# Performance work log

Hardware: AMD Instinct MI355X
Metric: run time of the kernel (lower is better)

Reference implementation:

```python
import jax, jax.numpy as jnp
import numpy as np

EPS = 1e-6
N_HEADS, N_KV = 16, 4


def rmsnorm(x, w):
    return x * jax.lax.rsqrt(jnp.mean(x * x, axis=-1, keepdims=True) + EPS) * w


def setup_inputs() -> dict:
    key = jax.random.key(0)
    ks = jax.random.split(key, 9)
    B, T, D, F = 2, 2048, 2048, 8192
    KVD = N_KV * (D // N_HEADS)
    s = lambda k, shape, fan: (jax.random.normal(k, shape, jnp.float32) * (fan ** -0.5))
    return {
        "x": jax.random.normal(ks[0], (B, T, D), jnp.float32),
        "norm1_w": jnp.ones((D,), jnp.float32),
        "norm2_w": jnp.ones((D,), jnp.float32),
        "Wq": s(ks[1], (D, D), D),
        "Wk": s(ks[2], (D, KVD), D),
        "Wv": s(ks[3], (D, KVD), D),
        "Wo": s(ks[4], (D, D), D),
        "Wc": s(ks[5], (D, D), D),
        "W1": s(ks[6], (D, F), D),
        "W2": s(ks[7], (F, D), F),
        "W3": s(ks[8], (D, F), D),
    }


def reference(x, norm1_w, norm2_w, Wq, Wk, Wv, Wo, Wc, W1, W2, W3):
    B, T, D = x.shape
    dh = D // N_HEADS          # 128
    G = N_HEADS // N_KV        # groups per kv head
    scale = dh ** -0.5

    xn = rmsnorm(x, norm1_w)
    q = xn @ Wq                               # [B,T,D]
    pos = q @ Wc                              # CoPE stand-in: contextual positional bias on Q
    q = (q + pos).reshape(B, T, N_KV, G, dh)  # group q heads under their kv head
    k = (xn @ Wk).reshape(B, T, N_KV, dh)
    v = (xn @ Wv).reshape(B, T, N_KV, dh)

    # GQA without repeat_interleave: contract each group against shared K/V
    scores = jnp.einsum('bqkgd,bskd->bkgqs', q, k) * scale   # [B,KV,G,T,T]
    i = jnp.arange(T)
    causal = i[:, None] >= i[None, :]
    scores = jnp.where(causal, scores, -jnp.inf)
    w = jax.nn.softmax(scores, axis=-1)
    att = jnp.einsum('bkgqs,bskd->bqkgd', w, v).reshape(B, T, D)

    x = x + att @ Wo
    xn2 = rmsnorm(x, norm2_w)
    x = x + (jax.nn.silu(xn2 @ W1) * (xn2 @ W3)) @ W2
    return x
```

## Files before the change

### kernel.cpp

```cpp
#include <hip/hip_runtime.h>
#include <hip/hip_bf16.h>

typedef __attribute__((ext_vector_type(8))) short short8;
typedef __attribute__((ext_vector_type(4))) float floatx4;
typedef unsigned short ushort_t;

__device__ inline float b2f(ushort_t s) {
    return __uint_as_float(((unsigned int)s) << 16);
}
__device__ inline ushort_t f2b(float f) {
    unsigned int u = __float_as_uint(f);
    unsigned int r = 0x7fff + ((u >> 16) & 1);
    return (ushort_t)((u + r) >> 16);
}
__device__ inline void load8(const float* p, float* f) {
    float4 a = *(const float4*)p;
    float4 b = *(const float4*)(p + 4);
    f[0] = a.x; f[1] = a.y; f[2] = a.z; f[3] = a.w;
    f[4] = b.x; f[5] = b.y; f[6] = b.z; f[7] = b.w;
}
__device__ inline void gload16(const ushort_t* g, ushort_t* l) {
    __builtin_amdgcn_global_load_lds(
        (const __attribute__((address_space(1))) unsigned int*)g,
        (__attribute__((address_space(3))) unsigned int*)l, 16, 0, 0);
}

__global__ __launch_bounds__(256) void transpose_w(const float* __restrict__ src,
                                                   ushort_t* __restrict__ dst,
                                                   int K, int N) {
    __shared__ ushort_t tile[64][65];
    int kb = blockIdx.x * 64, nb = blockIdx.y * 64;
    int t = threadIdx.x;
#pragma unroll
    for (int i = 0; i < 4; ++i) {
        int r = (t >> 4) + i * 16;
        int c = (t & 15) * 4;
        float4 v = *(const float4*)(src + (size_t)(kb + r) * N + nb + c);
        tile[c + 0][r] = f2b(v.x);
        tile[c + 1][r] = f2b(v.y);
        tile[c + 2][r] = f2b(v.z);
        tile[c + 3][r] = f2b(v.w);
    }
    __syncthreads();
#pragma unroll
    for (int i = 0; i < 2; ++i) {
        int s = t + i * 256;
        int n = s >> 3, kc = (s & 7) * 8;
        ushort_t o[8];
#pragma unroll
        for (int j = 0; j < 8; ++j) o[j] = tile[n][kc + j];
        *(uint4*)(dst + (size_t)(nb + n) * K + kb + kc) = *(const uint4*)o;
    }
}

__global__ __launch_bounds__(256) void rmsnorm_kernel(const float* __restrict__ x,
                                                      const float* __restrict__ w,
                                                      ushort_t* __restrict__ out, int D) {
    int row = blockIdx.x;
    int t = threadIdx.x;
    const float* xr = x + (size_t)row * D;
    float f[8];
    load8(xr + t * 8, f);
    float ss = 0.f;
#pragma unroll
    for (int i = 0; i < 8; ++i) ss += f[i] * f[i];
#pragma unroll
    for (int m = 1; m < 64; m <<= 1) ss += __shfl_xor(ss, m);
    __shared__ float wsum[4];
    if ((t & 63) == 0) wsum[t >> 6] = ss;
    __syncthreads();
    float tot = wsum[0] + wsum[1] + wsum[2] + wsum[3];
    float r = rsqrtf(tot / (float)D + 1e-6f);
    float wf[8];
    load8(w + t * 8, wf);
    ushort_t o[8];
#pragma unroll
    for (int i = 0; i < 8; ++i) o[i] = f2b(f[i] * r * wf[i]);
    *(uint4*)(out + (size_t)row * D + t * 8) = *(const uint4*)o;
}

__global__ __launch_bounds__(256) void reduce_out(const ushort_t* __restrict__ p,
                                                  const float* __restrict__ resid,
                                                  float* __restrict__ out, int n) {
    int stride = gridDim.x * 256;
    for (int i = blockIdx.x * 256 + threadIdx.x; i * 8 < n; i += stride) {
        int i8 = i * 8;
        uint4 a = *(const uint4*)(p + i8);
        uint4 b = *(const uint4*)(p + n + i8);
        const ushort_t* ae = (const ushort_t*)&a;
        const ushort_t* be = (const ushort_t*)&b;
        float rr[8];
        load8(resid + i8, rr);
        float o[8];
#pragma unroll
        for (int j = 0; j < 8; ++j) o[j] = b2f(ae[j]) + b2f(be[j]) + rr[j];
        *(float4*)(out + i8) = make_float4(o[0], o[1], o[2], o[3]);
        *(float4*)(out + i8 + 4) = make_float4(o[4], o[5], o[6], o[7]);
    }
}

__device__ inline void vm6() { asm volatile("s_waitcnt vmcnt(6)" ::: "memory"); }
__device__ inline void vm4() { asm volatile("s_waitcnt vmcnt(4)" ::: "memory"); }

template <int MODE>
__global__ __launch_bounds__(512, 2) void gemm8(const ushort_t* __restrict__ A,
                                                const ushort_t* __restrict__ Bt,
                                                const ushort_t* __restrict__ aux,
                                                const float* __restrict__ aux2,
                                                void* __restrict__ Cv,
                                                void* __restrict__ C2v,
                                                void* __restrict__ C3v,
                                                int M, int N, int Ksub, int lda) {
    __shared__ __align__(16) ushort_t Lds[2 * 32768];
    const int tid = threadIdx.x;
    const int wv = tid >> 6, lane = tid & 63;
    const int l16 = lane & 15, l4 = lane >> 4;
    const int wr = wv >> 2, wc = wv & 3;
    int nwg = gridDim.x;
    int per = nwg >> 3;
    int wg = (blockIdx.x & 7) * per + (blockIdx.x >> 3);
    int mtiles = M >> 8;
    int bx = wg & (mtiles - 1);
    int by = wg / mtiles;
    int bm = bx << 8, bn = by << 8;
    int koff = blockIdx.y * Ksub;

    const int sr = tid >> 3;
    const int scol = (((tid & 7) ^ (sr & 7)) << 3);
    const ushort_t* gA = A + (size_t)(bm + sr) * lda + scol + koff;
    const ushort_t* gB = Bt + (size_t)(bn + sr) * lda + scol + koff;
    ushort_t* ldsw = Lds + wv * 512;

    const int ktiles = Ksub >> 6;
    const int niter = ktiles >> 1;
    const int km = ktiles - 1;

#define STG_A(slot, j, kt) gload16(gA + (size_t)((j) * 64) * lda + ((kt) << 6), ldsw + (slot) * 32768 + (j) * 4096)
#define STG_B(slot, j, kt) gload16(gB + (size_t)((j) * 64) * lda + ((kt) << 6), ldsw + (slot) * 32768 + 16384 + (j) * 4096)

    STG_A(0, 0, 0); STG_A(0, 2, 0); STG_A(0, 1, 0); STG_A(0, 3, 0);
    STG_B(0, 0, 0); STG_B(0, 1, 0); STG_B(0, 2, 0); STG_B(0, 3, 0);
    STG_A(1, 0, 1); STG_A(1, 2, 1);
    STG_B(1, 0, 1); STG_B(1, 1, 1); STG_B(1, 2, 1); STG_B(1, 3, 1);
    vm6();
    asm volatile("" ::: "memory");
    __builtin_amdgcn_s_barrier();

    const int lx = l4 ^ (l16 & 7);
    floatx4 acc[8][4] = {};
    short8 aR[4][2], bR[4][2];

#define DSA(slot, mh) { _Pragma("unroll") for (int m = 0; m < 4; ++m) { \
    _Pragma("unroll") for (int kk = 0; kk < 2; ++kk) \
      aR[m][kk] = *(const short8*)(Lds + (slot) * 32768 + \
          (wr * 128 + (mh) * 64 + m * 16 + l16) * 64 + ((lx ^ (kk << 2)) << 3)); } }
#define DSB(slot, nh) { _Pragma("unroll") for (int n = 0; n < 2; ++n) { \
    _Pragma("unroll") for (int kk = 0; kk < 2; ++kk) \
      bR[(nh) * 2 + n][kk] = *(const short8*)(Lds + (slot) * 32768 + 16384 + \
          (wc * 64 + ((nh) * 2 + n) * 16 + l16) * 64 + ((lx ^ (kk << 2)) << 3)); } }
#define QUAD(mh, nlo) { _Pragma("unroll") for (int m = 0; m < 4; ++m) \
    _Pragma("unroll") for (int n = 0; n < 2; ++n) \
    _Pragma("unroll") for (int kk = 0; kk < 2; ++kk) \
      acc[(mh) * 4 + m][(nlo) + n] = __builtin_amdgcn_mfma_f32_16x16x32_bf16( \
          aR[m][kk], bR[(nlo) + n][kk], acc[(mh) * 4 + m][(nlo) + n], 0, 0, 0); }
#define PHASE(DS, ST, MH, NLO, VM) { \
    DS; ST; \
    asm volatile("" ::: "memory"); \
    __builtin_amdgcn_s_barrier(); \
    asm volatile("s_waitcnt lgkmcnt(0)" ::: "memory"); \
    __builtin_amdgcn_sched_barrier(0); \
    __builtin_amdgcn_s_setprio(1); \
    QUAD(MH, NLO); \
    __builtin_amdgcn_s_setprio(0); \
    VM; \
    asm volatile("" ::: "memory"); \
    __builtin_amdgcn_s_barrier(); }

    for (int it = 0; it < niter; ++it) {
        int t1 = 2 * it + 1;
        int t2 = (2 * it + 2) & km;
        int t3 = (2 * it + 3) & km;
        PHASE({ DSA(0, 0); DSB(0, 0); }, { STG_A(1, 1, t1); STG_A(1, 3, t1); }, 0, 0, );
        PHASE({ DSB(0, 1); },            { STG_A(0, 0, t2); STG_A(0, 2, t2); }, 0, 2, );
        PHASE({ DSA(0, 1); },            { STG_B(0, 0, t2); STG_B(0, 1, t2); }, 1, 2, );
        PHASE({ },                       { STG_B(0, 2, t2); STG_B(0, 3, t2); }, 1, 0, vm6(); );
        PHASE({ DSA(1, 0); DSB(1, 0); }, { STG_A(0, 1, t2); STG_A(0, 3, t2); }, 0, 0, );
        PHASE({ DSB(1, 1); },            { STG_A(1, 0, t3); STG_A(1, 2, t3); }, 0, 2, );
        PHASE({ DSA(1, 1); },            { STG_B(1, 0, t3); STG_B(1, 1, t3); }, 1, 2, );
        PHASE({ },                       { STG_B(1, 2, t3); STG_B(1, 3, t3); }, 1, 0, vm6(); );
    }

#pragma unroll
    for (int mi = 0; mi < 8; ++mi)
#pragma unroll
        for (int ni = 0; ni < 4; ++ni)
#pragma unroll
            for (int r = 0; r < 4; ++r) {
                int row = bm + wr * 128 + mi * 16 + l4 * 4 + r;
                int col = bn + wc * 64 + ni * 16 + l16;
                size_t idx = (size_t)row * N + col;
                float v = acc[mi][ni][r];
                if (MODE == 0) {
                    ((ushort_t*)Cv)[idx] = f2b(v);
                } else if (MODE == 1) {
                    ((ushort_t*)Cv)[idx] = f2b(v + b2f(aux[idx]));
                } else if (MODE == 2) {
                    float h = b2f(aux[idx]);
                    ((ushort_t*)Cv)[idx] = f2b((h / (1.f + __expf(-h))) * v);
                } else if (MODE == 3) {
                    ((ushort_t*)Cv)[(size_t)blockIdx.y * M * N + idx] = f2b(v);
                } else if (MODE == 5) {
                    ((float*)Cv)[idx] = v + aux2[idx];
                } else if (MODE == 6) {
                    if (bn < 2048) {
                        ((ushort_t*)Cv)[(size_t)row * 2048 + col] = f2b(v);
                    } else if (bn < 2560) {
                        ((ushort_t*)C2v)[(size_t)row * 512 + (col - 2048)] = f2b(v);
                    } else {
                        ((ushort_t*)C3v)[(size_t)(col - 2560) * 4096 + row] = f2b(v);
                    }
                }
            }
#undef STG_A
#undef STG_B
#undef DSA
#undef DSB
#undef QUAD
#undef PHASE
}

template <int MODE>
__global__ __launch_bounds__(512, 1) void gemm8h(const ushort_t* __restrict__ A,
                                                 const ushort_t* __restrict__ Bt,
                                                 const ushort_t* __restrict__ aux,
                                                 const float* __restrict__ aux2,
                                                 void* __restrict__ Cv,
                                                 int M, int N, int K) {
    __shared__ __align__(16) ushort_t Lds[2 * 24576];
    const int tid = threadIdx.x;
    const int wv = tid >> 6, lane = tid & 63;
    const int l16 = lane & 15, l4 = lane >> 4;
    const int wr = wv >> 2, wc = wv & 3;
    int nwg = gridDim.x;
    int per = nwg >> 3;
    int wg = (blockIdx.x & 7) * per + (blockIdx.x >> 3);
    int mtiles = M >> 7;
    int bx = wg & (mtiles - 1);
    int by = wg / mtiles;
    int bm = bx << 7, bn = by << 8;

    const int sr = tid >> 3;
    const int scol = (((tid & 7) ^ (sr & 7)) << 3);
    const ushort_t* gA = A + (size_t)(bm + sr) * K + scol;
    const ushort_t* gB = Bt + (size_t)(bn + sr) * K + scol;
    ushort_t* ldsw = Lds + wv * 512;

    const int ktiles = K >> 6;
    const int niter = ktiles >> 1;
    const int km = ktiles - 1;

#define HSTG_A(slot, j, kt) gload16(gA + (size_t)((j) * 64) * K + ((kt) << 6), ldsw + (slot) * 24576 + (j) * 4096)
#define HSTG_B(slot, j, kt) gload16(gB + (size_t)((j) * 64) * K + ((kt) << 6), ldsw + (slot) * 24576 + 8192 + (j) * 4096)

    HSTG_A(0, 0, 0); HSTG_A(0, 1, 0);
    HSTG_B(0, 0, 0); HSTG_B(0, 1, 0); HSTG_B(0, 2, 0); HSTG_B(0, 3, 0);
    HSTG_A(1, 0, 1); HSTG_A(1, 1, 1);
    HSTG_B(1, 0, 1); HSTG_B(1, 1, 1);
    vm4();
    asm volatile("" ::: "memory");
    __builtin_amdgcn_s_barrier();

    const int lx = l4 ^ (l16 & 7);
    floatx4 acc[4][4] = {};
    short8 aR[2][2], bR[4][2];

#define HDSA(slot, mh) { _Pragma("unroll") for (int m = 0; m < 2; ++m) { \
    _Pragma("unroll") for (int kk = 0; kk < 2; ++kk) \
      aR[m][kk] = *(const short8*)(Lds + (slot) * 24576 + \
          (wr * 64 + (mh) * 32 + m * 16 + l16) * 64 + ((lx ^ (kk << 2)) << 3)); } }
#define HDSB(slot, nh) { _Pragma("unroll") for (int n = 0; n < 2; ++n) { \
    _Pragma("unroll") for (int kk = 0; kk < 2; ++kk) \
      bR[(nh) * 2 + n][kk] = *(const short8*)(Lds + (slot) * 24576 + 8192 + \
          (wc * 64 + ((nh) * 2 + n) * 16 + l16) * 64 + ((lx ^ (kk << 2)) << 3)); } }
#define HQUAD(mh, nlo) { _Pragma("unroll") for (int m = 0; m < 2; ++m) \
    _Pragma("unroll") for (int n = 0; n < 2; ++n) \
    _Pragma("unroll") for (int kk = 0; kk < 2; ++kk) \
      acc[(mh) * 2 + m][(nlo) + n] = __builtin_amdgcn_mfma_f32_16x16x32_bf16( \
          aR[m][kk], bR[(nlo) + n][kk], acc[(mh) * 2 + m][(nlo) + n], 0, 0, 0); }
#define HPHASE(DS, ST, MH, NLO, VM) { \
    DS; ST; \
    asm volatile("" ::: "memory"); \
    __builtin_amdgcn_s_barrier(); \
    asm volatile("s_waitcnt lgkmcnt(0)" ::: "memory"); \
    __builtin_amdgcn_sched_barrier(0); \
    __builtin_amdgcn_s_setprio(1); \
    HQUAD(MH, NLO); \
    __builtin_amdgcn_s_setprio(0); \
    VM; \
    asm volatile("" ::: "memory"); \
    __builtin_amdgcn_s_barrier(); }

    for (int it = 0; it < niter; ++it) {
        int t1 = 2 * it + 1;
        int t2 = (2 * it + 2) & km;
        int t3 = (2 * it + 3) & km;
        HPHASE({ HDSA(0, 0); HDSB(0, 0); }, { HSTG_B(1, 2, t1); HSTG_B(1, 3, t1); }, 0, 0, );
        HPHASE({ HDSB(0, 1); },             { },                                     0, 2, );
        HPHASE({ HDSA(0, 1); },             { HSTG_B(0, 0, t2); HSTG_B(0, 1, t2); }, 1, 2, );
        HPHASE({ },                         { HSTG_B(0, 2, t2); HSTG_B(0, 3, t2); }, 1, 0, vm4(); );
        HPHASE({ HDSA(1, 0); HDSB(1, 0); }, { HSTG_A(0, 0, t2); HSTG_A(0, 1, t2); }, 0, 0, );
        HPHASE({ HDSB(1, 1); },             { },                                     0, 2, );
        HPHASE({ HDSA(1, 1); },             { HSTG_B(1, 0, t3); HSTG_B(1, 1, t3); }, 1, 2, );
        HPHASE({ },                         { HSTG_A(1, 0, t3); HSTG_A(1, 1, t3); }, 1, 0, vm4(); );
    }

#pragma unroll
    for (int mi = 0; mi < 4; ++mi)
#pragma unroll
        for (int ni = 0; ni < 4; ++ni)
#pragma unroll
            for (int r = 0; r < 4; ++r) {
                int row = bm + wr * 64 + mi * 16 + l4 * 4 + r;
                int col = bn + wc * 64 + ni * 16 + l16;
                size_t idx = (size_t)row * N + col;
                float v = acc[mi][ni][r];
                if (MODE == 1) ((ushort_t*)Cv)[idx] = f2b(v + b2f(aux[idx]));
                else if (MODE == 5) ((float*)Cv)[idx] = v + aux2[idx];
            }
#undef HSTG_A
#undef HSTG_B
#undef HDSA
#undef HDSB
#undef HQUAD
#undef HPHASE
}

#define QB 64
#define SB 64

__global__ __launch_bounds__(256, 2) void attn_kernel(const ushort_t* __restrict__ Q,
                                                      const ushort_t* __restrict__ Kb,
                                                      const ushort_t* __restrict__ VbT,
                                                      ushort_t* __restrict__ O, int Tlen) {
    const int D = 2048, KVD = 512, dh = 128;
    const int MTOK = 4096;
    int p = blockIdx.x, h = blockIdx.y, b = blockIdx.z;
    int kv = h >> 2;
    int t = threadIdx.x, wave = t >> 6, lane = t & 63;
    int l16 = lane & 15, l4 = lane >> 4;
    __shared__ __align__(16) ushort_t Ks[SB][dh + 8];
    __shared__ __align__(16) ushort_t Vt[dh][SB + 8];
    __shared__ __align__(16) ushort_t Ps[4][16][SB + 8];
    const float scale = 0.08838834764831845f;
    const ushort_t* Kg = Kb + ((size_t)(b * Tlen) + (t >> 4)) * KVD + kv * dh + (t & 15) * 8;
    const ushort_t* Vg = VbT + (size_t)(kv * dh + (t >> 3)) * MTOK + b * Tlen + (t & 7) * 8;

    for (int side = 0; side < 2; ++side) {
        int qt = side ? p : (31 - p);
        int qbase = qt * QB;
        int qfrag = qbase + wave * 16;
        short8 qf[4];
        const ushort_t* Qrow = Q + ((size_t)(b * Tlen) + qfrag + l16) * D + h * dh;
#pragma unroll
        for (int kk = 0; kk < 4; ++kk) qf[kk] = *(const short8*)(Qrow + kk * 32 + l4 * 8);
        floatx4 o_acc[8] = {};
        float m_r[4], l_r[4];
#pragma unroll
        for (int r = 0; r < 4; ++r) { m_r[r] = -INFINITY; l_r[r] = 0.f; }
        int nst = qt + 1;
        uint4 kreg[4], vreg[4];
#pragma unroll
        for (int p4 = 0; p4 < 4; ++p4) {
            kreg[p4] = *(const uint4*)(Kg + (size_t)(p4 * 16) * KVD);
            vreg[p4] = *(const uint4*)(Vg + (size_t)(p4 * 32) * MTOK);
        }
        for (int st = 0; st < nst; ++st) {
            __syncthreads();
#pragma unroll
            for (int p4 = 0; p4 < 4; ++p4) {
                *(uint4*)(&Ks[(t >> 4) + p4 * 16][(t & 15) * 8]) = kreg[p4];
                *(uint4*)(&Vt[(t >> 3) + p4 * 32][(t & 7) * 8]) = vreg[p4];
            }
            __syncthreads();
            if (st + 1 < nst) {
                size_t off = (size_t)(st + 1) * SB;
#pragma unroll
                for (int p4 = 0; p4 < 4; ++p4) {
                    kreg[p4] = *(const uint4*)(Kg + (off + p4 * 16) * KVD);
                    vreg[p4] = *(const uint4*)(Vg + (size_t)(p4 * 32) * MTOK + off);
                }
            }
            int s0 = st * SB;
            floatx4 sa[4] = {};
            __builtin_amdgcn_s_setprio(1);
#pragma unroll
            for (int ss = 0; ss < 4; ++ss)
#pragma unroll
                for (int kk = 0; kk < 4; ++kk) {
                    short8 kf = *(const short8*)(&Ks[ss * 16 + l16][kk * 32 + l4 * 8]);
                    sa[ss] = __builtin_amdgcn_mfma_f32_16x16x32_bf16(qf[kk], kf, sa[ss], 0, 0, 0);
                }
            __builtin_amdgcn_s_setprio(0);
            float sv[4][4], pmax[4];
#pragma unroll
            for (int r = 0; r < 4; ++r) pmax[r] = -INFINITY;
#pragma unroll
            for (int ss = 0; ss < 4; ++ss) {
                int scol = s0 + ss * 16 + l16;
#pragma unroll
                for (int r = 0; r < 4; ++r) {
                    int qrow = qfrag + l4 * 4 + r;
                    float v = sa[ss][r] * scale;
                    if (scol > qrow) v = -INFINITY;
                    sv[ss][r] = v;
                    pmax[r] = fmaxf(pmax[r], v);
                }
            }
#pragma unroll
            for (int m = 1; m < 16; m <<= 1)
#pragma unroll
                for (int r = 0; r < 4; ++r) pmax[r] = fmaxf(pmax[r], __shfl_xor(pmax[r], m));
            int cflag = 1;
#pragma unroll
            for (int r = 0; r < 4; ++r) cflag &= (pmax[r] <= m_r[r] + 8.f) ? 1 : 0;
            bool skip = __all(cflag);
            float mn[4], rsum[4];
#pragma unroll
            for (int r = 0; r < 4; ++r) {
                mn[r] = skip ? m_r[r] : fmaxf(m_r[r], pmax[r]);
                rsum[r] = 0.f;
            }
#pragma unroll
            for (int ss = 0; ss < 4; ++ss)
#pragma unroll
                for (int r = 0; r < 4; ++r) {
                    float pv = __expf(sv[ss][r] - mn[r]);
                    sv[ss][r] = pv;
                    rsum[r] += pv;
                }
#pragma unroll
            for (int m = 1; m < 16; m <<= 1)
#pragma unroll
                for (int r = 0; r < 4; ++r) rsum[r] += __shfl_xor(rsum[r], m);
            if (skip) {
#pragma unroll
                for (int r = 0; r < 4; ++r) l_r[r] += rsum[r];
            } else {
#pragma unroll
                for (int r = 0; r < 4; ++r) {
                    float esc = __expf(m_r[r] - mn[r]);
                    l_r[r] = l_r[r] * esc + rsum[r];
                    m_r[r] = mn[r];
#pragma unroll
                    for (int c = 0; c < 8; ++c) o_acc[c][r] *= esc;
                }
            }
#pragma unroll
            for (int ss = 0; ss < 4; ++ss)
#pragma unroll
                for (int r = 0; r < 4; ++r)
                    Ps[wave][l4 * 4 + r][ss * 16 + l16] = f2b(sv[ss][r]);
            short8 pa[2];
#pragma unroll
            for (int kk = 0; kk < 2; ++kk)
                pa[kk] = *(const short8*)(&Ps[wave][l16][kk * 32 + l4 * 8]);
            __builtin_amdgcn_s_setprio(1);
#pragma unroll
            for (int c = 0; c < 8; ++c)
#pragma unroll
                for (int kk = 0; kk < 2; ++kk) {
                    short8 vf = *(const short8*)(&Vt[c * 16 + l16][kk * 32 + l4 * 8]);
                    o_acc[c] = __builtin_amdgcn_mfma_f32_16x16x32_bf16(pa[kk], vf, o_acc[c], 0, 0, 0);
                }
            __builtin_amdgcn_s_setprio(0);
        }
        __syncthreads();
        ushort_t* Osh = &Ks[0][0];
#pragma unroll
        for (int c = 0; c < 8; ++c)
#pragma unroll
            for (int r = 0; r < 4; ++r)
                Osh[(wave * 16 + l4 * 4 + r) * 136 + c * 16 + l16] = f2b(o_acc[c][r] / l_r[r]);
        __syncthreads();
        {
            int orow = t >> 2, occ = (t & 3) * 32;
            const ushort_t* srcp = Osh + orow * 136 + occ;
            ushort_t* dstp = O + ((size_t)(b * Tlen) + qbase + orow) * D + h * dh + occ;
#pragma unroll
            for (int k = 0; k < 4; ++k)
                *(uint4*)(dstp + k * 8) = *(const uint4*)(srcp + k * 8);
        }
    }
}

extern "C" void kernel_launch(void* const* d_in, const int* in_sizes, int n_in,
                              void* d_out, int out_size, void* d_ws, size_t ws_size,
                              hipStream_t stream) {
    const float* x   = (const float*)d_in[0];
    const float* n1w = (const float*)d_in[1];
    const float* n2w = (const float*)d_in[2];
    const float* Wq  = (const float*)d_in[3];
    const float* Wk  = (const float*)d_in[4];
    const float* Wv  = (const float*)d_in[5];
    const float* Wo  = (const float*)d_in[6];
    const float* Wc  = (const float*)d_in[7];
    const float* W1  = (const float*)d_in[8];
    const float* W2  = (const float*)d_in[9];
    const float* W3  = (const float*)d_in[10];
    float* out = (float*)d_out;

    const int B = 2, T = 2048, D = 2048, F = 8192, KVD = 512;
    const int M = B * T;
    const size_t XD   = (size_t)M * D * 2;
    const size_t XDF  = (size_t)M * D * 4;
    const size_t KVSZ = (size_t)M * KVD * 2;
    const size_t MF   = (size_t)M * F * 2;
    const size_t WDD  = (size_t)D * D * 2;
    const size_t WQKV = (size_t)(D + 2 * KVD) * D * 2;
    const size_t WDF  = (size_t)D * F * 2;

    char* w = (char*)d_ws;
    ushort_t* xn    = (ushort_t*)(w);
    ushort_t* qtmp  = (ushort_t*)(w + XD);
    ushort_t* qfin  = (ushort_t*)(w + 2 * XD);
    float*    x2f   = (float*)   (w + 3 * XD);
    ushort_t* kbuf  = (ushort_t*)(w + 3 * XD + XDF);
    ushort_t* vbufT = (ushort_t*)(w + 3 * XD + XDF + KVSZ);
    ushort_t* h1    = (ushort_t*)(w + 3 * XD + XDF + 2 * KVSZ);
    char* wt = w + 3 * XD + XDF + 2 * KVSZ + MF;
    ushort_t* WqkvT = (ushort_t*)(wt);
    ushort_t* WcT   = (ushort_t*)(wt + WQKV);
    ushort_t* WoT   = (ushort_t*)(wt + WQKV + WDD);
    ushort_t* W1T   = (ushort_t*)(wt + WQKV + 2 * WDD);
    ushort_t* W3T   = (ushort_t*)(wt + WQKV + 2 * WDD + WDF);
    ushort_t* W2T   = (ushort_t*)(wt + WQKV + 2 * WDD + 2 * WDF);

    dim3 blk(256);
    dim3 blk8(512);

    transpose_w<<<dim3(D / 64, D / 64), blk, 0, stream>>>(Wq, WqkvT, D, D);
    transpose_w<<<dim3(D / 64, KVD / 64), blk, 0, stream>>>(Wk, WqkvT + (size_t)2048 * D, D, KVD);
    transpose_w<<<dim3(D / 64, KVD / 64), blk, 0, stream>>>(Wv, WqkvT + (size_t)2560 * D, D, KVD);
    transpose_w<<<dim3(D / 64, D / 64), blk, 0, stream>>>(Wc, WcT, D, D);
    transpose_w<<<dim3(D / 64, D / 64), blk, 0, stream>>>(Wo, WoT, D, D);
    transpose_w<<<dim3(D / 64, F / 64), blk, 0, stream>>>(W1, W1T, D, F);
    transpose_w<<<dim3(D / 64, F / 64), blk, 0, stream>>>(W3, W3T, D, F);
    transpose_w<<<dim3(F / 64, D / 64), blk, 0, stream>>>(W2, W2T, F, D);

    rmsnorm_kernel<<<M, blk, 0, stream>>>(x, n1w, xn, D);
    gemm8<6><<<dim3((M / 256) * (3072 / 256)), blk8, 0, stream>>>(
        xn, WqkvT, nullptr, nullptr, qtmp, kbuf, vbufT, M, 3072, D, D);
    gemm8h<1><<<dim3((M / 128) * (D / 256)), blk8, 0, stream>>>(
        qtmp, WcT, qtmp, nullptr, qfin, M, D, D);
    attn_kernel<<<dim3(16, 16, B), blk, 0, stream>>>(qfin, kbuf, vbufT, qtmp, T);
    gemm8h<5><<<dim3((M / 128) * (D / 256)), blk8, 0, stream>>>(
        qtmp, WoT, nullptr, x, x2f, M, D, D);
    rmsnorm_kernel<<<M, blk, 0, stream>>>(x2f, n2w, xn, D);
    gemm8<0><<<dim3((M / 256) * (F / 256)), blk8, 0, stream>>>(
        xn, W1T, nullptr, nullptr, h1, nullptr, nullptr, M, F, D, D);
    gemm8<2><<<dim3((M / 256) * (F / 256)), blk8, 0, stream>>>(
        xn, W3T, h1, nullptr, h1, nullptr, nullptr, M, F, D, D);
    gemm8<3><<<dim3((M / 256) * (D / 256), 2), blk8, 0, stream>>>(
        h1, W2T, nullptr, nullptr, xn, nullptr, nullptr, M, D, F / 2, F);
    reduce_out<<<1024, blk, 0, stream>>>(xn, x2f, out, M * D);
}
```

Baseline: 837.2 us.

## Process paired causal q-tiles together in attention and merge weight transposes

The attention kernel now handles the high and low query tiles of each block in one pass over K/V, so each K/V tile is loaded into LDS once and used for both query tiles while they overlap. This removes the second K/V streaming pass and doubles the MFMA work per loaded tile, at the cost of more registers (two sets of accumulators and Q fragments) and a larger P buffer in shared memory. Separately, the eight weight-transpose launches are merged into one kernel that dispatches on block index, which cuts launch overhead.

After: 851.0 us. Within noise of the previous version (+1.7%).

```diff
diff --git a/kernel.cpp b/kernel.cpp
--- a/kernel.cpp
+++ b/kernel.cpp
@@ -25,11 +25,26 @@
         (__attribute__((address_space(3))) unsigned int*)l, 16, 0, 0);
 }
 
-__global__ __launch_bounds__(256) void transpose_w(const float* __restrict__ src,
-                                                   ushort_t* __restrict__ dst,
-                                                   int K, int N) {
+__global__ __launch_bounds__(256) void transpose_all(
+    const float* __restrict__ s0, const float* __restrict__ s1,
+    const float* __restrict__ s2, const float* __restrict__ s3,
+    const float* __restrict__ s4, const float* __restrict__ s5,
+    const float* __restrict__ s6, const float* __restrict__ s7,
+    ushort_t* d0, ushort_t* d1, ushort_t* d2, ushort_t* d3,
+    ushort_t* d4, ushort_t* d5, ushort_t* d6, ushort_t* d7) {
+    int id = blockIdx.x;
+    const float* src; ushort_t* dst; int K, N;
+    if (id < 1024)       { src = s0; dst = d0; K = 2048; N = 2048; }
+    else if (id < 1280)  { id -= 1024;  src = s1; dst = d1; K = 2048; N = 512; }
+    else if (id < 1536)  { id -= 1280;  src = s2; dst = d2; K = 2048; N = 512; }
+    else if (id < 2560)  { id -= 1536;  src = s3; dst = d3; K = 2048; N = 2048; }
+    else if (id < 3584)  { id -= 2560;  src = s4; dst = d4; K = 2048; N = 2048; }
+    else if (id < 7680)  { id -= 3584;  src = s5; dst = d5; K = 2048; N = 8192; }
+    else if (id < 11776) { id -= 7680;  src = s6; dst = d6; K = 2048; N = 8192; }
+    else                 { id -= 11776; src = s7; dst = d7; K = 8192; N = 2048; }
+    int tn = N >> 6;
+    int kb = (id / tn) * 64, nb = (id % tn) * 64;
     __shared__ ushort_t tile[64][65];
-    int kb = blockIdx.x * 64, nb = blockIdx.y * 64;
     int t = threadIdx.x;
 #pragma unroll
     for (int i = 0; i < 4; ++i) {
@@ -338,6 +353,56 @@
 #define QB 64
 #define SB 64
 
+#define SOFTMAX_SIDE(sacc, m_r, l_r, o_acc, qfrag, psr)                         \
+    {                                                                           \
+        float sv[4][4], pmax[4];                                                \
+        _Pragma("unroll") for (int r = 0; r < 4; ++r) pmax[r] = -INFINITY;      \
+        _Pragma("unroll") for (int ss = 0; ss < 4; ++ss) {                      \
+            int scol = s0 + ss * 16 + l16;                                      \
+            _Pragma("unroll") for (int r = 0; r < 4; ++r) {                     \
+                int qrow = (qfrag) + l4 * 4 + r;                                \
+                float v = sacc[ss][r] * scale;                                  \
+                if (scol > qrow) v = -INFINITY;                                 \
+                sv[ss][r] = v;                                                  \
+                pmax[r] = fmaxf(pmax[r], v);                                    \
+            }                                                                   \
+        }                                                                       \
+        _Pragma("unroll") for (int m = 1; m < 16; m <<= 1)                      \
+            _Pragma("unroll") for (int r = 0; r < 4; ++r)                       \
+                pmax[r] = fmaxf(pmax[r], __shfl_xor(pmax[r], m));               \
+        int cflag = 1;                                                          \
+        _Pragma("unroll") for (int r = 0; r < 4; ++r)                           \
+            cflag &= (pmax[r] <= m_r[r] + 8.f) ? 1 : 0;                         \
+        bool skip = __all(cflag);                                               \
+        float mn[4], rsum[4];                                                   \
+        _Pragma("unroll") for (int r = 0; r < 4; ++r) {                         \
+            mn[r] = skip ? m_r[r] : fmaxf(m_r[r], pmax[r]);                     \
+            rsum[r] = 0.f;                                                      \
+        }                                                                       \
+        _Pragma("unroll") for (int ss = 0; ss < 4; ++ss)                        \
+            _Pragma("unroll") for (int r = 0; r < 4; ++r) {                     \
+                float pv = __expf(sv[ss][r] - mn[r]);                           \
+                sv[ss][r] = pv;                                                 \
+                rsum[r] += pv;                                                  \
+            }                                                                   \
+        _Pragma("unroll") for (int m = 1; m < 16; m <<= 1)                      \
+            _Pragma("unroll") for (int r = 0; r < 4; ++r)                       \
+                rsum[r] += __shfl_xor(rsum[r], m);                              \
+        if (skip) {                                                             \
+            _Pragma("unroll") for (int r = 0; r < 4; ++r) l_r[r] += rsum[r];    \
+        } else {                                                                \
+            _Pragma("unroll") for (int r = 0; r < 4; ++r) {                     \
+                float esc = __expf(m_r[r] - mn[r]);                             \
+                l_r[r] = l_r[r] * esc + rsum[r];                                \
+                m_r[r] = mn[r];                                                 \
+                _Pragma("unroll") for (int c = 0; c < 8; ++c) o_acc[c][r] *= esc; \
+            }                                                                   \
+        }                                                                       \
+        _Pragma("unroll") for (int ss = 0; ss < 4; ++ss)                        \
+            _Pragma("unroll") for (int r = 0; r < 4; ++r)                       \
+                Ps[psr][l4 * 4 + r][ss * 16 + l16] = f2b(sv[ss][r]);            \
+    }
+
 __global__ __launch_bounds__(256, 2) void attn_kernel(const ushort_t* __restrict__ Q,
                                                       const ushort_t* __restrict__ Kb,
                                                       const ushort_t* __restrict__ VbT,
@@ -350,146 +415,137 @@
     int l16 = lane & 15, l4 = lane >> 4;
     __shared__ __align__(16) ushort_t Ks[SB][dh + 8];
     __shared__ __align__(16) ushort_t Vt[dh][SB + 8];
-    __shared__ __align__(16) ushort_t Ps[4][16][SB + 8];
+    __shared__ __align__(16) ushort_t Ps[8][16][SB + 8];
     const float scale = 0.08838834764831845f;
     const ushort_t* Kg = Kb + ((size_t)(b * Tlen) + (t >> 4)) * KVD + kv * dh + (t & 15) * 8;
     const ushort_t* Vg = VbT + (size_t)(kv * dh + (t >> 3)) * MTOK + b * Tlen + (t & 7) * 8;
 
-    for (int side = 0; side < 2; ++side) {
-        int qt = side ? p : (31 - p);
-        int qbase = qt * QB;
-        int qfrag = qbase + wave * 16;
-        short8 qf[4];
-        const ushort_t* Qrow = Q + ((size_t)(b * Tlen) + qfrag + l16) * D + h * dh;
-#pragma unroll
-        for (int kk = 0; kk < 4; ++kk) qf[kk] = *(const short8*)(Qrow + kk * 32 + l4 * 8);
-        floatx4 o_acc[8] = {};
-        float m_r[4], l_r[4];
-#pragma unroll
-        for (int r = 0; r < 4; ++r) { m_r[r] = -INFINITY; l_r[r] = 0.f; }
-        int nst = qt + 1;
-        uint4 kreg[4], vreg[4];
+    int qt_hi = 31 - p, qt_lo = p;
+    int qbase_hi = qt_hi * QB, qbase_lo = qt_lo * QB;
+    int qfrag_hi = qbase_hi + wave * 16;
+    int qfrag_lo = qbase_lo + wave * 16;
+    short8 qh[4], ql[4];
+    {
+        const ushort_t* Qh = Q + ((size_t)(b * Tlen) + qfrag_hi + l16) * D + h * dh;
+        const ushort_t* Ql = Q + ((size_t)(b * Tlen) + qfrag_lo + l16) * D + h * dh;
+#pragma unroll
+        for (int kk = 0; kk < 4; ++kk) {
+            qh[kk] = *(const short8*)(Qh + kk * 32 + l4 * 8);
+            ql[kk] = *(const short8*)(Ql + kk * 32 + l4 * 8);
+        }
+    }
+    floatx4 oh[8] = {}, ol[8] = {};
+    float mh[4], lh[4], ml[4], ll[4];
+#pragma unroll
+    for (int r = 0; r < 4; ++r) { mh[r] = -INFINITY; lh[r] = 0.f; ml[r] = -INFINITY; ll[r] = 0.f; }
+    int nst = qt_hi + 1;
+    uint4 kreg[4], vreg[4];
+#pragma unroll
+    for (int p4 = 0; p4 < 4; ++p4) {
+        kreg[p4] = *(const uint4*)(Kg + (size_t)(p4 * 16) * KVD);
+        vreg[p4] = *(const uint4*)(Vg + (size_t)(p4 * 32) * MTOK);
+    }
+    for (int st = 0; st < nst; ++st) {
+        __syncthreads();
 #pragma unroll
         for (int p4 = 0; p4 < 4; ++p4) {
-            kreg[p4] = *(const uint4*)(Kg + (size_t)(p4 * 16) * KVD);
-            vreg[p4] = *(const uint4*)(Vg + (size_t)(p4 * 32) * MTOK);
+            *(uint4*)(&Ks[(t >> 4) + p4 * 16][(t & 15) * 8]) = kreg[p4];
+            *(uint4*)(&Vt[(t >> 3) + p4 * 32][(t & 7) * 8]) = vreg[p4];
         }
-        for (int st = 0; st < nst; ++st) {
-            __syncthreads();
+        __syncthreads();
+        if (st + 1 < nst) {
+            size_t off = (size_t)(st + 1) * SB;
 #pragma unroll
             for (int p4 = 0; p4 < 4; ++p4) {
-                *(uint4*)(&Ks[(t >> 4) + p4 * 16][(t & 15) * 8]) = kreg[p4];
-                *(uint4*)(&Vt[(t >> 3) + p4 * 32][(t & 7) * 8]) = vreg[p4];
+                kreg[p4] = *(const uint4*)(Kg + (off + p4 * 16) * KVD);
+                vreg[p4] = *(const uint4*)(Vg + (size_t)(p4 * 32) * MTOK + off);
             }
-            __syncthreads();
-            if (st + 1 < nst) {
-                size_t off = (size_t)(st + 1) * SB;
-#pragma unroll
-                for (int p4 = 0; p4 < 4; ++p4) {
-                    kreg[p4] = *(const uint4*)(Kg + (off + p4 * 16) * KVD);
-                    vreg[p4] = *(const uint4*)(Vg + (size_t)(p4 * 32) * MTOK + off);
-                }
-            }
-            int s0 = st * SB;
-            floatx4 sa[4] = {};
-            __builtin_amdgcn_s_setprio(1);
+        }
+        int s0 = st * SB;
+        bool dual = (st <= qt_lo);
+        floatx4 sh[4] = {}, sl[4] = {};
+        __builtin_amdgcn_s_setprio(1);
+        if (dual) {
 #pragma unroll
             for (int ss = 0; ss < 4; ++ss)
 #pragma unroll
                 for (int kk = 0; kk < 4; ++kk) {
                     short8 kf = *(const short8*)(&Ks[ss * 16 + l16][kk * 32 + l4 * 8]);
-                    sa[ss] = __builtin_amdgcn_mfma_f32_16x16x32_bf16(qf[kk], kf, sa[ss], 0, 0, 0);
+                    sh[ss] = __builtin_amdgcn_mfma_f32_16x16x32_bf16(qh[kk], kf, sh[ss], 0, 0, 0);
+                    sl[ss] = __builtin_amdgcn_mfma_f32_16x16x32_bf16(ql[kk], kf, sl[ss], 0, 0, 0);
                 }
-            __builtin_amdgcn_s_setprio(0);
-            float sv[4][4], pmax[4];
-#pragma unroll
-            for (int r = 0; r < 4; ++r) pmax[r] = -INFINITY;
-#pragma unroll
-            for (int ss = 0; ss < 4; ++ss) {
-                int scol = s0 + ss * 16 + l16;
-#pragma unroll
-                for (int r = 0; r < 4; ++r) {
-                    int qrow = qfrag + l4 * 4 + r;
-                    float v = sa[ss][r] * scale;
-                    if (scol > qrow) v = -INFINITY;
-                    sv[ss][r] = v;
-                    pmax[r] = fmaxf(pmax[r], v);
+        } else {
+#pragma unroll
+            for (int ss = 0; ss < 4; ++ss)
+#pragma unroll
+                for (int kk = 0; kk < 4; ++kk) {
+                    short8 kf = *(const short8*)(&Ks[ss * 16 + l16][kk * 32 + l4 * 8]);
+                    sh[ss] = __builtin_amdgcn_mfma_f32_16x16x32_bf16(qh[kk], kf, sh[ss], 0, 0, 0);
                 }
-            }
-#pragma unroll
-            for (int m = 1; m < 16; m <<= 1)
-#pragma unroll
-                for (int r = 0; r < 4; ++r) pmax[r] = fmaxf(pmax[r], __shfl_xor(pmax[r], m));
-            int cflag = 1;
-#pragma unroll
-            for (int r = 0; r < 4; ++r) cflag &= (pmax[r] <= m_r[r] + 8.f) ? 1 : 0;
-            bool skip = __all(cflag);
-            float mn[4], rsum[4];
-#pragma unroll
-            for (int r = 0; r < 4; ++r) {
-                mn[r] = skip ? m_r[r] : fmaxf(m_r[r], pmax[r]);
-                rsum[r] = 0.f;
-            }
-#pragma unroll
-            for (int ss = 0; ss < 4; ++ss)
-#pragma unroll
-                for (int r = 0; r < 4; ++r) {
-                    float pv = __expf(sv[ss][r] - mn[r]);
-                    sv[ss][r] = pv;
-                    rsum[r] += pv;
-                }
-#pragma unroll
-            for (int m = 1; m < 16; m <<= 1)
-#pragma unroll
-                for (int r = 0; r < 4; ++r) rsum[r] += __shfl_xor(rsum[r], m);
-            if (skip) {
-#pragma unroll
-                for (int r = 0; r < 4; ++r) l_r[r] += rsum[r];
-            } else {
-#pragma unroll
-                for (int r = 0; r < 4; ++r) {
-                    float esc = __expf(m_r[r] - mn[r]);
-                    l_r[r] = l_r[r] * esc + rsum[r];
-                    m_r[r] = mn[r];
-#pragma unroll
-                    for (int c = 0; c < 8; ++c) o_acc[c][r] *= esc;
-                }
-            }
-#pragma unroll
-            for (int ss = 0; ss < 4; ++ss)
-#pragma unroll
-                for (int r = 0; r < 4; ++r)
-                    Ps[wave][l4 * 4 + r][ss * 16 + l16] = f2b(sv[ss][r]);
-            short8 pa[2];
+        }
+        __builtin_amdgcn_s_setprio(0);
+        SOFTMAX_SIDE(sh, mh, lh, oh, qfrag_hi, wave)
+        if (dual) SOFTMAX_SIDE(sl, ml, ll, ol, qfrag_lo, wave + 4)
+        short8 pah[2], pal[2];
+#pragma unroll
+        for (int kk = 0; kk < 2; ++kk)
+            pah[kk] = *(const short8*)(&Ps[wave][l16][kk * 32 + l4 * 8]);
+        if (dual) {
 #pragma unroll
             for (int kk = 0; kk < 2; ++kk)
-                pa[kk] = *(const short8*)(&Ps[wave][l16][kk * 32 + l4 * 8]);
-            __builtin_amdgcn_s_setprio(1);
+                pal[kk] = *(const short8*)(&Ps[wave + 4][l16][kk * 32 + l4 * 8]);
+        }
+        __builtin_amdgcn_s_setprio(1);
+        if (dual) {
 #pragma unroll
             for (int c = 0; c < 8; ++c)
 #pragma unroll
                 for (int kk = 0; kk < 2; ++kk) {
                     short8 vf = *(const short8*)(&Vt[c * 16 + l16][kk * 32 + l4 * 8]);
-                    o_acc[c] = __builtin_amdgcn_mfma_f32_16x16x32_bf16(pa[kk], vf, o_acc[c], 0, 0, 0);
+                    oh[c] = __builtin_amdgcn_mfma_f32_16x16x32_bf16(pah[kk], vf, oh[c], 0, 0, 0);
+                    ol[c] = __builtin_amdgcn_mfma_f32_16x16x32_bf16(pal[kk], vf, ol[c], 0, 0, 0);
                 }
-            __builtin_amdgcn_s_setprio(0);
+        } else {
+#pragma unroll
+            for (int c = 0; c < 8; ++c)
+#pragma unroll
+                for (int kk = 0; kk < 2; ++kk) {
+                    short8 vf = *(const short8*)(&Vt[c * 16 + l16][kk * 32 + l4 * 8]);
+                    oh[c] = __builtin_amdgcn_mfma_f32_16x16x32_bf16(pah[kk], vf, oh[c], 0, 0, 0);
+                }
         }
-        __syncthreads();
-        ushort_t* Osh = &Ks[0][0];
-#pragma unroll
-        for (int c = 0; c < 8; ++c)
-#pragma unroll
-            for (int r = 0; r < 4; ++r)
-                Osh[(wave * 16 + l4 * 4 + r) * 136 + c * 16 + l16] = f2b(o_acc[c][r] / l_r[r]);
-        __syncthreads();
-        {
-            int orow = t >> 2, occ = (t & 3) * 32;
-            const ushort_t* srcp = Osh + orow * 136 + occ;
-            ushort_t* dstp = O + ((size_t)(b * Tlen) + qbase + orow) * D + h * dh + occ;
-#pragma unroll
-            for (int k = 0; k < 4; ++k)
-                *(uint4*)(dstp + k * 8) = *(const uint4*)(srcp + k * 8);
-        }
+        __builtin_amdgcn_s_setprio(0);
+    }
+    ushort_t* Osh = &Ks[0][0];
+    __syncthreads();
+#pragma unroll
+    for (int c = 0; c < 8; ++c)
+#pragma unroll
+        for (int r = 0; r < 4; ++r)
+            Osh[(wave * 16 + l4 * 4 + r) * 136 + c * 16 + l16] = f2b(oh[c][r] / lh[r]);
+    __syncthreads();
+    {
+        int orow = t >> 2, occ = (t & 3) * 32;
+        const ushort_t* srcp = Osh + orow * 136 + occ;
+        ushort_t* dstp = O + ((size_t)(b * Tlen) + qbase_hi + orow) * D + h * dh + occ;
+#pragma unroll
+        for (int k = 0; k < 4; ++k)
+            *(uint4*)(dstp + k * 8) = *(const uint4*)(srcp + k * 8);
+    }
+    __syncthreads();
+#pragma unroll
+    for (int c = 0; c < 8; ++c)
+#pragma unroll
+        for (int r = 0; r < 4; ++r)
+            Osh[(wave * 16 + l4 * 4 + r) * 136 + c * 16 + l16] = f2b(ol[c][r] / ll[r]);
+    __syncthreads();
+    {
+        int orow = t >> 2, occ = (t & 3) * 32;
+        const ushort_t* srcp = Osh + orow * 136 + occ;
+        ushort_t* dstp = O + ((size_t)(b * Tlen) + qbase_lo + orow) * D + h * dh + occ;
+#pragma unroll
+        for (int k = 0; k < 4; ++k)
+            *(uint4*)(dstp + k * 8) = *(const uint4*)(srcp + k * 8);
     }
 }
 
@@ -538,14 +594,10 @@
     dim3 blk(256);
     dim3 blk8(512);
 
-    transpose_w<<<dim3(D / 64, D / 64), blk, 0, stream>>>(Wq, WqkvT, D, D);
-    transpose_w<<<dim3(D / 64, KVD / 64), blk, 0, stream>>>(Wk, WqkvT + (size_t)2048 * D, D, KVD);
-    transpose_w<<<dim3(D / 64, KVD / 64), blk, 0, stream>>>(Wv, WqkvT + (size_t)2560 * D, D, KVD);
-    transpose_w<<<dim3(D / 64, D / 64), blk, 0, stream>>>(Wc, WcT, D, D);
-    transpose_w<<<dim3(D / 64, D / 64), blk, 0, stream>>>(Wo, WoT, D, D);
-    transpose_w<<<dim3(D / 64, F / 64), blk, 0, stream>>>(W1, W1T, D, F);
-    transpose_w<<<dim3(D / 64, F / 64), blk, 0, stream>>>(W3, W3T, D, F);
-    transpose_w<<<dim3(F / 64, D / 64), blk, 0, stream>>>(W2, W2T, F, D);
+    transpose_all<<<15872, blk, 0, stream>>>(
+        Wq, Wk, Wv, Wc, Wo, W1, W3, W2,
+        WqkvT, WqkvT + (size_t)2048 * D, WqkvT + (size_t)2560 * D,
+        WcT, WoT, W1T, W3T, W2T);
 
     rmsnorm_kernel<<<M, blk, 0, stream>>>(x, n1w, xn, D);
     gemm8<6><<<dim3((M / 256) * (3072 / 256)), blk8, 0, stream>>>(
```

## Double-buffer attention K/V tiles in LDS and merge weight transposes into one launch

Applied to the files above, without the earlier changes.

The attention kernel now keeps two LDS buffers for K and V. The next tile is written into the other buffer while the current one is used for compute, so each iteration needs one barrier instead of two. The eight weight-transpose launches are also merged into a single kernel that works out which matrix a block handles from its block index, which removes per-launch overhead and tail gaps. The extra LDS roughly doubles K/V shared memory and may limit occupancy for the launch_bounds(256,2) attention kernel.

Result: faster. 810.3 us (-3.2%).

```diff
diff --git a/kernel.cpp b/kernel.cpp
--- a/kernel.cpp
+++ b/kernel.cpp
@@ -25,11 +25,26 @@
         (__attribute__((address_space(3))) unsigned int*)l, 16, 0, 0);
 }
 
-__global__ __launch_bounds__(256) void transpose_w(const float* __restrict__ src,
-                                                   ushort_t* __restrict__ dst,
-                                                   int K, int N) {
+__global__ __launch_bounds__(256) void transpose_all(
+    const float* __restrict__ s0, const float* __restrict__ s1,
+    const float* __restrict__ s2, const float* __restrict__ s3,
+    const float* __restrict__ s4, const float* __restrict__ s5,
+    const float* __restrict__ s6, const float* __restrict__ s7,
+    ushort_t* d0, ushort_t* d1, ushort_t* d2, ushort_t* d3,
+    ushort_t* d4, ushort_t* d5, ushort_t* d6, ushort_t* d7) {
+    int id = blockIdx.x;
+    const float* src; ushort_t* dst; int K, N;
+    if (id < 1024)       { src = s0; dst = d0; K = 2048; N = 2048; }
+    else if (id < 1280)  { id -= 1024;  src = s1; dst = d1; K = 2048; N = 512; }
+    else if (id < 1536)  { id -= 1280;  src = s2; dst = d2; K = 2048; N = 512; }
+    else if (id < 2560)  { id -= 1536;  src = s3; dst = d3; K = 2048; N = 2048; }
+    else if (id < 3584)  { id -= 2560;  src = s4; dst = d4; K = 2048; N = 2048; }
+    else if (id < 7680)  { id -= 3584;  src = s5; dst = d5; K = 2048; N = 8192; }
+    else if (id < 11776) { id -= 7680;  src = s6; dst = d6; K = 2048; N = 8192; }
+    else                 { id -= 11776; src = s7; dst = d7; K = 8192; N = 2048; }
+    int tn = N >> 6;
+    int kb = (id / tn) * 64, nb = (id % tn) * 64;
     __shared__ ushort_t tile[64][65];
-    int kb = blockIdx.x * 64, nb = blockIdx.y * 64;
     int t = threadIdx.x;
 #pragma unroll
     for (int i = 0; i < 4; ++i) {
@@ -348,8 +363,8 @@
     int kv = h >> 2;
     int t = threadIdx.x, wave = t >> 6, lane = t & 63;
     int l16 = lane & 15, l4 = lane >> 4;
-    __shared__ __align__(16) ushort_t Ks[SB][dh + 8];
-    __shared__ __align__(16) ushort_t Vt[dh][SB + 8];
+    __shared__ __align__(16) ushort_t Ks[2][SB][dh + 8];
+    __shared__ __align__(16) ushort_t Vt[2][dh][SB + 8];
     __shared__ __align__(16) ushort_t Ps[4][16][SB + 8];
     const float scale = 0.08838834764831845f;
     const ushort_t* Kg = Kb + ((size_t)(b * Tlen) + (t >> 4)) * KVD + kv * dh + (t & 15) * 8;
@@ -374,33 +389,48 @@
             kreg[p4] = *(const uint4*)(Kg + (size_t)(p4 * 16) * KVD);
             vreg[p4] = *(const uint4*)(Vg + (size_t)(p4 * 32) * MTOK);
         }
+        __syncthreads();
+#pragma unroll
+        for (int p4 = 0; p4 < 4; ++p4) {
+            *(uint4*)(&Ks[0][(t >> 4) + p4 * 16][(t & 15) * 8]) = kreg[p4];
+            *(uint4*)(&Vt[0][(t >> 3) + p4 * 32][(t & 7) * 8]) = vreg[p4];
+        }
+        if (nst > 1) {
+#pragma unroll
+            for (int p4 = 0; p4 < 4; ++p4) {
+                kreg[p4] = *(const uint4*)(Kg + (size_t)(SB + p4 * 16) * KVD);
+                vreg[p4] = *(const uint4*)(Vg + (size_t)(p4 * 32) * MTOK + SB);
+            }
+        }
+        __syncthreads();
         for (int st = 0; st < nst; ++st) {
-            __syncthreads();
-#pragma unroll
-            for (int p4 = 0; p4 < 4; ++p4) {
-                *(uint4*)(&Ks[(t >> 4) + p4 * 16][(t & 15) * 8]) = kreg[p4];
-                *(uint4*)(&Vt[(t >> 3) + p4 * 32][(t & 7) * 8]) = vreg[p4];
-            }
-            __syncthreads();
+            int cur = st & 1;
+            int s0 = st * SB;
+            floatx4 sa[4] = {};
+            __builtin_amdgcn_s_setprio(1);
+#pragma unroll
+            for (int ss = 0; ss < 4; ++ss)
+#pragma unroll
+                for (int kk = 0; kk < 4; ++kk) {
+                    short8 kf = *(const short8*)(&Ks[cur][ss * 16 + l16][kk * 32 + l4 * 8]);
+                    sa[ss] = __builtin_amdgcn_mfma_f32_16x16x32_bf16(qf[kk], kf, sa[ss], 0, 0, 0);
+                }
+            __builtin_amdgcn_s_setprio(0);
             if (st + 1 < nst) {
-                size_t off = (size_t)(st + 1) * SB;
+#pragma unroll
+                for (int p4 = 0; p4 < 4; ++p4) {
+                    *(uint4*)(&Ks[cur ^ 1][(t >> 4) + p4 * 16][(t & 15) * 8]) = kreg[p4];
+                    *(uint4*)(&Vt[cur ^ 1][(t >> 3) + p4 * 32][(t & 7) * 8]) = vreg[p4];
+                }
+            }
+            if (st + 2 < nst) {
+                size_t off = (size_t)(st + 2) * SB;
 #pragma unroll
                 for (int p4 = 0; p4 < 4; ++p4) {
                     kreg[p4] = *(const uint4*)(Kg + (off + p4 * 16) * KVD);
                     vreg[p4] = *(const uint4*)(Vg + (size_t)(p4 * 32) * MTOK + off);
                 }
             }
-            int s0 = st * SB;
-            floatx4 sa[4] = {};
-            __builtin_amdgcn_s_setprio(1);
-#pragma unroll
-            for (int ss = 0; ss < 4; ++ss)
-#pragma unroll
-                for (int kk = 0; kk < 4; ++kk) {
-                    short8 kf = *(const short8*)(&Ks[ss * 16 + l16][kk * 32 + l4 * 8]);
-                    sa[ss] = __builtin_amdgcn_mfma_f32_16x16x32_bf16(qf[kk], kf, sa[ss], 0, 0, 0);
-                }
-            __builtin_amdgcn_s_setprio(0);
             float sv[4][4], pmax[4];
 #pragma unroll
             for (int r = 0; r < 4; ++r) pmax[r] = -INFINITY;
@@ -469,13 +499,13 @@
             for (int c = 0; c < 8; ++c)
 #pragma unroll
                 for (int kk = 0; kk < 2; ++kk) {
-                    short8 vf = *(const short8*)(&Vt[c * 16 + l16][kk * 32 + l4 * 8]);
+                    short8 vf = *(const short8*)(&Vt[cur][c * 16 + l16][kk * 32 + l4 * 8]);
                     o_acc[c] = __builtin_amdgcn_mfma_f32_16x16x32_bf16(pa[kk], vf, o_acc[c], 0, 0, 0);
                 }
             __builtin_amdgcn_s_setprio(0);
+            __syncthreads();
         }
-        __syncthreads();
-        ushort_t* Osh = &Ks[0][0];
+        ushort_t* Osh = &Ks[0][0][0];
 #pragma unroll
         for (int c = 0; c < 8; ++c)
 #pragma unroll
@@ -538,14 +568,10 @@
     dim3 blk(256);
     dim3 blk8(512);
 
-    transpose_w<<<dim3(D / 64, D / 64), blk, 0, stream>>>(Wq, WqkvT, D, D);
-    transpose_w<<<dim3(D / 64, KVD / 64), blk, 0, stream>>>(Wk, WqkvT + (size_t)2048 * D, D, KVD);
-    transpose_w<<<dim3(D / 64, KVD / 64), blk, 0, stream>>>(Wv, WqkvT + (size_t)2560 * D, D, KVD);
-    transpose_w<<<dim3(D / 64, D / 64), blk, 0, stream>>>(Wc, WcT, D, D);
-    transpose_w<<<dim3(D / 64, D / 64), blk, 0, stream>>>(Wo, WoT, D, D);
-    transpose_w<<<dim3(D / 64, F / 64), blk, 0, stream>>>(W1, W1T, D, F);
-    transpose_w<<<dim3(D / 64, F / 64), blk, 0, stream>>>(W3, W3T, D, F);
-    transpose_w<<<dim3(F / 64, D / 64), blk, 0, stream>>>(W2, W2T, F, D);
+    transpose_all<<<15872, blk, 0, stream>>>(
+        Wq, Wk, Wv, Wc, Wo, W1, W3, W2,
+        WqkvT, WqkvT + (size_t)2048 * D, WqkvT + (size_t)2560 * D,
+        WcT, WoT, W1T, W3T, W2T);
 
     rmsnorm_kernel<<<M, blk, 0, stream>>>(x, n1w, xn, D);
     gemm8<6><<<dim3((M / 256) * (3072 / 256)), blk8, 0, stream>>>(
```
